# Kernel optimization log

Hardware: AMD Instinct MI355X
Metric: run time of the kernel (lower is better)

## Reference

```python
import jax, jax.numpy as jnp
import numpy as np

B, T, C = 2, 2048, 1024
H, DH = 16, 64          # n_heads = d_model // 64
WIN = 256               # sliding window size
K = 32                  # n_oscillators
DFF = 4096              # d_ff_hidden
NEG = -1e9


def setup_inputs() -> dict:
    key = jax.random.key(0)
    ks = jax.random.split(key, 16)
    sC = 1.0 / np.sqrt(C)
    sF = 1.0 / np.sqrt(DFF)
    sK = 1.0 / np.sqrt(K)
    return {
        "x": jax.random.normal(ks[0], (B, T, C), jnp.float32),
        "norm1_w": jnp.ones((C,), jnp.float32),
        "qkv_w": jax.random.normal(ks[1], (3 * C, C), jnp.float32) * sC,
        "qkv_b": jnp.zeros((3 * C,), jnp.float32),
        "proj_w": jax.random.normal(ks[2], (C, C), jnp.float32) * sC,
        "proj_b": jnp.zeros((C,), jnp.float32),
        "gate_w": jax.random.normal(ks[3], (1, C), jnp.float32) * 0.01,
        "gate_b": jnp.zeros((1,), jnp.float32),
        "trn_win": jax.random.normal(ks[4], (K, C), jnp.float32) * sC,
        "trn_wout": jax.random.normal(ks[5], (C, K), jnp.float32) * sK,
        "trn_gate_w": jax.random.normal(ks[6], (K, C), jnp.float32) * sC,
        "trn_gate_b": jnp.zeros((K,), jnp.float32),
        "trn_a_logit": jax.random.normal(ks[7], (K,), jnp.float32),
        "trn_theta": jax.random.uniform(ks[8], (K,), jnp.float32, 0.0, np.pi),
        "trn_res_scale": jnp.asarray(0.1, jnp.float32),
        "norm2_w": jnp.ones((C,), jnp.float32),
        "ffn_gate_w": jax.random.normal(ks[9], (DFF, C), jnp.float32) * sC,
        "ffn_up_w": jax.random.normal(ks[10], (DFF, C), jnp.float32) * sC,
        "ffn_down_w": jax.random.normal(ks[11], (C, DFF), jnp.float32) * sF,
    }


def _rms(z, w, eps=1e-6):
    return z * jax.lax.rsqrt(jnp.mean(z * z, axis=-1, keepdims=True) + eps) * w


def reference(x, norm1_w, qkv_w, qkv_b, proj_w, proj_b, gate_w, gate_b,
              trn_win, trn_wout, trn_gate_w, trn_gate_b, trn_a_logit,
              trn_theta, trn_res_scale, norm2_w, ffn_gate_w, ffn_up_w,
              ffn_down_w):
    h = _rms(x, norm1_w)

    # ---- windowed causal attention (dense mask, as in the original) ----
    qkv = h @ qkv_w.T + qkv_b                       # [B,T,3C]
    q, k, v = jnp.split(qkv, 3, axis=-1)
    heads = lambda t: t.reshape(B, T, H, DH).transpose(0, 2, 1, 3)  # [B,H,T,DH]
    q, k, v = heads(q), heads(k), heads(v)
    row = jnp.arange(T)[:, None]
    col = jnp.arange(T)[None, :]
    mask = jnp.where((col <= row) & (col >= row - WIN + 1), 0.0, NEG).astype(x.dtype)
    scores = jnp.einsum('bhqd,bhkd->bhqk', q, k) / jnp.sqrt(jnp.asarray(DH, x.dtype))
    attn = jax.nn.softmax(scores + mask, axis=-1)
    ao = jnp.einsum('bhqk,bhkd->bhqd', attn, v).transpose(0, 2, 1, 3).reshape(B, T, C)
    ao = ao @ proj_w.T + proj_b

    # ---- temporal resonance branch: K damped rotating oscillators ----
    u = h @ trn_win.T                               # [B,T,K] drive
    a = jax.nn.sigmoid(trn_a_logit)                 # amplitude in (0,1) (amplitude_max=1)
    ct, st = jnp.cos(trn_theta), jnp.sin(trn_theta)

    def step(carry, ut):
        sr, si = carry
        nsr = a * (ct * sr - st * si) + ut
        nsi = a * (st * sr + ct * si)
        return (nsr, nsi), nsr

    init = (jnp.zeros((B, K), x.dtype), jnp.zeros((B, K), x.dtype))
    _, ys = jax.lax.scan(step, init, u.transpose(1, 0, 2))  # ys: [T,B,K]
    y = ys.transpose(1, 0, 2)                                # [B,T,K]
    tg = jax.nn.sigmoid(h @ trn_gate_w.T + trn_gate_b)
    trn_out = ((tg * y) @ trn_wout.T) * trn_res_scale        # [B,T,C]

    # ---- sigmoid gate mix + residual ----
    g = jax.nn.sigmoid(h @ gate_w.T + gate_b)       # [B,T,1]
    x = x + g * ao + (1.0 - g) * trn_out

    # ---- SwiGLU FFN ----
    h2 = _rms(x, norm2_w)
    ffn = (jax.nn.silu(h2 @ ffn_gate_w.T) * (h2 @ ffn_up_w.T)) @ ffn_down_w.T
    return x + ffn
```

## Files before the change

### kernel.cpp

```cpp
#include <hip/hip_runtime.h>


typedef unsigned short u16;
typedef unsigned short u16x8 __attribute__((ext_vector_type(8)));
typedef __bf16 bf16x8 __attribute__((ext_vector_type(8)));
typedef float f32x4 __attribute__((ext_vector_type(4)));

#define DI static __device__ __forceinline__

DI u16 f2b(float f){
  union { float f; unsigned u; } v; v.f = f;
  unsigned r = v.u + 0x7FFFu + ((v.u >> 16) & 1u);
  return (u16)(r >> 16);
}
DI float b2f(u16 b){
  union { unsigned u; float f; } v; v.u = ((unsigned)b) << 16; return v.f;
}
DI u16x8 ld8(const u16* p){ return *(const u16x8*)p; }

DI f32x4 MFMA16(u16x8 a, u16x8 b, f32x4 c){
  return __builtin_amdgcn_mfma_f32_16x16x32_bf16(
      __builtin_bit_cast(bf16x8, a), __builtin_bit_cast(bf16x8, b), c, 0, 0, 0);
}

DI void async16(const void* g, void* l){
  void* gg = const_cast<void*>(g);
  __builtin_amdgcn_global_load_lds(
      (__attribute__((address_space(1))) void*)gg,
      (__attribute__((address_space(3))) void*)l, 16, 0, 0);
}

__global__ __launch_bounds__(256) void prep_kernel(
    const float* __restrict__ qkvw, const float* __restrict__ projw,
    const float* __restrict__ fgw, const float* __restrict__ fuw,
    const float* __restrict__ fdw, const float* __restrict__ twin,
    const float* __restrict__ tgw, const float* __restrict__ twout,
    u16* __restrict__ dst,
    const float* __restrict__ x, const float* __restrict__ n1w,
    const float* __restrict__ gw, const float* __restrict__ gb,
    u16* __restrict__ h, float* __restrict__ g)
{
  const int blk = blockIdx.x, tid = threadIdx.x;
  if (blk < 16640){
    size_t i = (size_t)blk * 256 + tid;
    if (i >= 4259840u) return;
    size_t e = i * 4;
    float4 v;
    if (e < 3145728u)        v = *(const float4*)(qkvw + e);
    else if (e < 3276800u){
      size_t i2 = e - 3145728u;
      int row = (int)(i2 >> 10), c = (int)(i2 & 1023);
      if (row < 32)      v = *(const float4*)(twin + row * 1024 + c);
      else if (row < 64) v = *(const float4*)(tgw + (row - 32) * 1024 + c);
      else               v = make_float4(0.f, 0.f, 0.f, 0.f);
    }
    else if (e < 4456448u){
      unsigned i2 = (unsigned)(e - 3276800u);
      unsigned row = i2 / 1152u, kk = i2 - row * 1152u;
      if (kk < 1024u)      v = *(const float4*)(projw + (size_t)row * 1024 + kk);
      else if (kk < 1056u) v = *(const float4*)(twout + (size_t)row * 32 + (kk - 1024u));
      else                 v = make_float4(0.f, 0.f, 0.f, 0.f);
    }
    else if (e < 12845056u){
      size_t i2 = e - 4456448u;
      int row = (int)(i2 >> 10), c = (int)(i2 & 1023);
      int G = row >> 5, j = row & 31;
      const float* src = (j < 16) ? fgw : fuw;
      v = *(const float4*)(src + (size_t)(G * 16 + (j & 15)) * 1024 + c);
    }
    else                   v = *(const float4*)(fdw + (e - 12845056u));
    uint2 p;
    p.x = (unsigned)f2b(v.x) | ((unsigned)f2b(v.y) << 16);
    p.y = (unsigned)f2b(v.z) | ((unsigned)f2b(v.w) << 16);
    *(uint2*)(dst + e) = p;
    return;
  }
  const int row = blk - 16640;
  const int wave = tid >> 6, lane = tid & 63;
  __shared__ float sb[8];
  float4 xv = ((const float4*)(x + (size_t)row * 1024))[tid];
  float ss = xv.x*xv.x + xv.y*xv.y + xv.z*xv.z + xv.w*xv.w;
#pragma unroll
  for (int m = 32; m; m >>= 1) ss += __shfl_xor(ss, m);
  if (lane == 0) sb[wave] = ss;
  __syncthreads();
  float rstd = rsqrtf((sb[0]+sb[1]+sb[2]+sb[3]) * (1.f/1024.f) + 1e-6f);
  float4 wv = ((const float4*)n1w)[tid];
  float h0 = xv.x*rstd*wv.x, h1 = xv.y*rstd*wv.y;
  float h2v = xv.z*rstd*wv.z, h3 = xv.w*rstd*wv.w;
  uint2 pk;
  pk.x = (unsigned)f2b(h0) | ((unsigned)f2b(h1) << 16);
  pk.y = (unsigned)f2b(h2v) | ((unsigned)f2b(h3) << 16);
  ((uint2*)(h + (size_t)row * 1024))[tid] = pk;
  float4 gv = ((const float4*)gw)[tid];
  float gd = h0*gv.x + h1*gv.y + h2v*gv.z + h3*gv.w;
#pragma unroll
  for (int m = 32; m; m >>= 1) gd += __shfl_xor(gd, m);
  if (lane == 0) sb[4 + wave] = gd;
  __syncthreads();
  if (tid == 0) g[row] = 1.f / (1.f + __expf(-(sb[4]+sb[5]+sb[6]+sb[7] + gb[0])));
}

__global__ __launch_bounds__(256) void reduce_mix_norm(
    const u16* __restrict__ part, const float* __restrict__ x,
    const float* __restrict__ g, const float* __restrict__ pb,
    const float* __restrict__ n2w,
    float* __restrict__ out, u16* __restrict__ h2)
{
  const int row = blockIdx.x, tid = threadIdx.x;
  const int wave = tid >> 6, lane = tid & 63;
  __shared__ float sb[4];
  const size_t ro = (size_t)row * 1024;
  uint2 a0 = ((const uint2*)(part + ro))[tid];
  uint2 a1 = ((const uint2*)(part + 4194304 + ro))[tid];
  float4 bb = ((const float4*)pb)[tid];
  float4 xv = ((const float4*)(x + ro))[tid];
  float gg = g[row];
  float m0 = xv.x + b2f((u16)a0.x) + b2f((u16)a1.x) + gg*bb.x;
  float m1 = xv.y + b2f((u16)(a0.x >> 16)) + b2f((u16)(a1.x >> 16)) + gg*bb.y;
  float m2 = xv.z + b2f((u16)a0.y) + b2f((u16)a1.y) + gg*bb.z;
  float m3 = xv.w + b2f((u16)(a0.y >> 16)) + b2f((u16)(a1.y >> 16)) + gg*bb.w;
  float4 mo; mo.x = m0; mo.y = m1; mo.z = m2; mo.w = m3;
  ((float4*)(out + ro))[tid] = mo;
  float ss = m0*m0 + m1*m1 + m2*m2 + m3*m3;
#pragma unroll
  for (int m = 32; m; m >>= 1) ss += __shfl_xor(ss, m);
  if (lane == 0) sb[wave] = ss;
  __syncthreads();
  float rstd = rsqrtf((sb[0]+sb[1]+sb[2]+sb[3]) * (1.f/1024.f) + 1e-6f);
  float4 wv = ((const float4*)n2w)[tid];
  uint2 pk;
  pk.x = (unsigned)f2b(m0*rstd*wv.x) | ((unsigned)f2b(m1*rstd*wv.y) << 16);
  pk.y = (unsigned)f2b(m2*rstd*wv.z) | ((unsigned)f2b(m3*rstd*wv.w) << 16);
  ((uint2*)(h2 + ro))[tid] = pk;
}

__global__ __launch_bounds__(256) void reduce_down(
    const u16* __restrict__ part, float* __restrict__ out)
{
  size_t i = (size_t)blockIdx.x * 256 + threadIdx.x;
  uint2 a0 = ((const uint2*)part)[i];
  uint2 a1 = ((const uint2*)(part + 4194304))[i];
  uint2 a2 = ((const uint2*)(part + 8388608))[i];
  uint2 a3 = ((const uint2*)(part + 12582912))[i];
  float4 xv = ((float4*)out)[i];
  float4 o;
  o.x = xv.x + b2f((u16)a0.x) + b2f((u16)a1.x) + b2f((u16)a2.x) + b2f((u16)a3.x);
  o.y = xv.y + b2f((u16)(a0.x >> 16)) + b2f((u16)(a1.x >> 16))
             + b2f((u16)(a2.x >> 16)) + b2f((u16)(a3.x >> 16));
  o.z = xv.z + b2f((u16)a0.y) + b2f((u16)a1.y) + b2f((u16)a2.y) + b2f((u16)a3.y);
  o.w = xv.w + b2f((u16)(a0.y >> 16)) + b2f((u16)(a1.y >> 16))
             + b2f((u16)(a2.y >> 16)) + b2f((u16)(a3.y >> 16));
  ((float4*)out)[i] = o;
}

template<int MODE>
__global__ __launch_bounds__(256) void gemm_bt(
    const u16* __restrict__ A, const u16* __restrict__ B,
    float* __restrict__ outF, float* __restrict__ outF2, u16* __restrict__ outB,
    const float* __restrict__ bias, const float* __restrict__ auxF,
    int M, int N, int K)
{
  __shared__ __align__(16) u16 sA[2][128 * 32];
  __shared__ __align__(16) u16 sB[2][128 * 32];
  const int tid = threadIdx.x;
  const int wave = tid >> 6, lane = tid & 63;
  const int lr = lane & 15, lq = lane >> 4;
  const int m0 = blockIdx.x * 128, n0 = blockIdx.y * 128;
  const int wm = (wave & 1) * 64, wn = (wave >> 1) * 64;
  const int ks = K / (int)gridDim.z;
  const int kbeg = (int)blockIdx.z * ks, kend = kbeg + ks;
  f32x4 acc[4][4] = {};
  const int srow = wave * 16 + (lane >> 2);
  const int scol = (lane & 3) * 8;
  const u16* gA = A + (size_t)(m0 + srow) * K + scol;
  const u16* gB = B + (size_t)(n0 + srow) * K + scol;
  u16* lA0 = &sA[0][(wave * 16) * 32];
  u16* lA1 = &sA[0][(64 + wave * 16) * 32];
  u16* lB0 = &sB[0][(wave * 16) * 32];
  u16* lB1 = &sB[0][(64 + wave * 16) * 32];
  const size_t K64 = (size_t)64 * K;
  const int BUF = 128 * 32;

  for (int k0 = kbeg; k0 < kend; k0 += 64){
    async16(gA + k0,            lA0);
    async16(gA + K64 + k0,      lA1);
    async16(gB + k0,            lB0);
    async16(gB + K64 + k0,      lB1);
    async16(gA + k0 + 32,       lA0 + BUF);
    async16(gA + K64 + k0 + 32, lA1 + BUF);
    async16(gB + k0 + 32,       lB0 + BUF);
    async16(gB + K64 + k0 + 32, lB1 + BUF);
    __syncthreads();
#pragma unroll
    for (int buf = 0; buf < 2; buf++){
      u16x8 af[4], bf[4];
#pragma unroll
      for (int i = 0; i < 4; i++) af[i] = ld8(&sA[buf][(wm + i*16 + lr)*32 + lq*8]);
#pragma unroll
      for (int i = 0; i < 4; i++) bf[i] = ld8(&sB[buf][(wn + i*16 + lr)*32 + lq*8]);
#pragma unroll
      for (int mi = 0; mi < 4; mi++)
#pragma unroll
        for (int ni = 0; ni < 4; ni++)
          acc[mi][ni] = MFMA16(af[mi], bf[ni], acc[mi][ni]);
    }
    __syncthreads();
  }

  if (MODE == 7){
    const int cb = ((n0 + wn) >> 1) + lr;
#pragma unroll
    for (int mi = 0; mi < 4; mi++){
      const int row = m0 + wm + mi*16 + lq*4;
#pragma unroll
      for (int p = 0; p < 2; p++){
        const int col = cb + p*16;
#pragma unroll
        for (int r = 0; r < 4; r++){
          float gv = acc[mi][2*p][r], uv = acc[mi][2*p+1][r];
          float rv = gv / (1.f + __expf(-gv)) * uv;
          outB[(size_t)(row + r) * (N >> 1) + col] = f2b(rv);
        }
      }
    }
    return;
  }

#pragma unroll
  for (int mi = 0; mi < 4; mi++){
    const int row = m0 + wm + mi*16 + lq*4;
#pragma unroll
    for (int ni = 0; ni < 4; ni++){
      const int col = n0 + wn + ni*16 + lr;
#pragma unroll
      for (int r = 0; r < 4; r++){
        const int rr = row + r;
        float v = acc[mi][ni][r];
        if (MODE == 0){
          if (n0 < 3072){
            outB[(size_t)rr * 3072 + col] = f2b(v + bias[col]);
          } else {
            int c2 = col - 3072;
            int bb = rr >> 11, tt = rr & 2047;
            if (c2 < 32) outF[((size_t)bb * 32 + c2) * 2048 + tt] = v;
            else if (c2 < 64)
              outF2[(size_t)rr * 32 + (c2 - 32)] =
                  1.f / (1.f + __expf(-(v + auxF[c2 - 32])));
          }
        } else if (MODE == 9){
          outB[(size_t)blockIdx.z * (size_t)M + (size_t)rr * N + col] = f2b(v);
        }
      }
    }
  }
}

__global__ __launch_bounds__(256) void attn_scan(
    const u16* __restrict__ qkv, const float* __restrict__ g,
    const float* __restrict__ u_t, const float* __restrict__ tg,
    const float* __restrict__ alog, const float* __restrict__ theta,
    const float* __restrict__ tscale, u16* __restrict__ Ap)
{
  __shared__ __align__(16) u16 sVt[64 * 72];
  __shared__ __align__(16) u16 sP[4][16 * 72];
  __shared__ float4 sc[256];
  const int blk = blockIdx.x, tid = threadIdx.x;

  if (blk < 1024){
    const int tile = blk & 31, hh = (blk >> 5) & 15, b = blk >> 9;
    const int t0 = tile * 64;
    const int wave = tid >> 6, lane = tid & 63;
    const int lr = lane & 15, lq = lane >> 4;
    const int qt = t0 + wave * 16;

    const u16* base = qkv + (size_t)b * 2048 * 3072 + hh * 64;
    const u16* qrow = base + (size_t)(qt + lr) * 3072 + lq * 8;
    u16x8 qf0 = ld8(qrow), qf1 = ld8(qrow + 32);
    const u16* kbase = base + 1024;
    const u16* vbase = base + 2048;

    f32x4 o0 = {0,0,0,0}, o1 = {0,0,0,0}, o2 = {0,0,0,0}, o3 = {0,0,0,0};
    float lsum[4] = {0.f, 0.f, 0.f, 0.f};
    const float c1 = 0.125f * 1.44269504088896f;

    const int kb = (t0 >= 256) ? (t0 - 256) : 0;
    const int ntl = (t0 + 64 - kb) >> 6;
    for (int it = 0; it < ntl; ++it){
      const int kt = kb + it * 64;
      __syncthreads();
      {
        const int key = tid & 63, dseg = tid >> 6;
        const u16* gv = vbase + (size_t)(kt + key) * 3072 + dseg * 16;
        u16x8 v0 = ld8(gv), v1 = ld8(gv + 8);
#pragma unroll
        for (int j = 0; j < 8; j++){
          sVt[(dseg*16 + j)     * 72 + key] = v0[j];
          sVt[(dseg*16 + 8 + j) * 72 + key] = v1[j];
        }
      }
      __syncthreads();
      const bool active = (kt < qt + 16) && (kt + 318 >= qt);
      if (!active) continue;

      f32x4 s[4] = {};
#pragma unroll
      for (int gK = 0; gK < 4; gK++){
        const u16* kr = kbase + (size_t)(kt + gK*16 + lr) * 3072 + lq * 8;
        u16x8 k0 = ld8(kr), k1 = ld8(kr + 32);
        s[gK] = MFMA16(qf0, k0, s[gK]);
        s[gK] = MFMA16(qf1, k1, s[gK]);
      }
#pragma unroll
      for (int r = 0; r < 4; r++){
        const int q = qt + lq * 4 + r;
#pragma unroll
        for (int gK = 0; gK < 4; gK++){
          const int c = kt + gK*16 + lr;
          float p = (c <= q && c + 255 >= q) ? exp2f(s[gK][r] * c1) : 0.f;
          lsum[r] += p;
          sP[wave][(lq*4 + r) * 72 + gK*16 + lr] = f2b(p);
        }
      }
      __builtin_amdgcn_s_waitcnt(0xc07f);
      u16x8 pf0 = ld8(&sP[wave][lr * 72 + lq * 8]);
      u16x8 pf1 = ld8(&sP[wave][lr * 72 + 32 + lq * 8]);
      o0 = MFMA16(pf0, ld8(&sVt[(lr)      * 72 + lq * 8]), o0);
      o0 = MFMA16(pf1, ld8(&sVt[(lr)      * 72 + 32 + lq * 8]), o0);
      o1 = MFMA16(pf0, ld8(&sVt[(16 + lr) * 72 + lq * 8]), o1);
      o1 = MFMA16(pf1, ld8(&sVt[(16 + lr) * 72 + 32 + lq * 8]), o1);
      o2 = MFMA16(pf0, ld8(&sVt[(32 + lr) * 72 + lq * 8]), o2);
      o2 = MFMA16(pf1, ld8(&sVt[(32 + lr) * 72 + 32 + lq * 8]), o2);
      o3 = MFMA16(pf0, ld8(&sVt[(48 + lr) * 72 + lq * 8]), o3);
      o3 = MFMA16(pf1, ld8(&sVt[(48 + lr) * 72 + 32 + lq * 8]), o3);
    }

#pragma unroll
    for (int r = 0; r < 4; r++){
      float l = lsum[r];
      l += __shfl_xor(l, 1); l += __shfl_xor(l, 2);
      l += __shfl_xor(l, 4); l += __shfl_xor(l, 8);
      lsum[r] = l;
    }

    const int trow = b * 2048 + qt + lq * 4;
    u16* aor = Ap + (size_t)trow * 1152 + hh * 64 + lr;
#pragma unroll
    for (int r = 0; r < 4; r++){
      float inv = g[trow + r] / lsum[r];
      u16* p = aor + (size_t)r * 1152;
      p[0]  = f2b(o0[r] * inv);
      p[16] = f2b(o1[r] * inv);
      p[32] = f2b(o2[r] * inv);
      p[48] = f2b(o3[r] * inv);
    }
    return;
  }

  if (blk < 1088){
    const int bk = blk - 1024;
    const int b = bk >> 5, k = bk & 31;
    const int j = tid;
    const float a = 1.f / (1.f + __expf(-alog[k]));
    const float th = theta[k];
    const float rs = tscale[0];
    const float wr = a * __cosf(th), wi = a * __sinf(th);
    const float* ubp = u_t + ((size_t)b * 32 + k) * 2048 + j * 8;
    float4 ua = ((const float4*)ubp)[0];
    float4 ub4 = ((const float4*)ubp)[1];
    float ur[8] = {ua.x, ua.y, ua.z, ua.w, ub4.x, ub4.y, ub4.z, ub4.w};
    float sr = 0.f, si = 0.f;
#pragma unroll
    for (int i = 0; i < 8; i++){
      float nr = wr*sr - wi*si + ur[i];
      float ni = wi*sr + wr*si;
      sr = nr; si = ni;
    }
    float w2r = wr*wr - wi*wi, w2i = 2.f*wr*wi;
    float w4r = w2r*w2r - w2i*w2i, w4i = 2.f*w2r*w2i;
    float Ar = w4r*w4r - w4i*w4i, Ai = 2.f*w4r*w4i;
    float4 cur; cur.x = Ar; cur.y = Ai; cur.z = sr; cur.w = si;
    sc[j] = cur;
    __syncthreads();
    for (int s = 1; s < 256; s <<= 1){
      float4 pv;
      const bool has = (j >= s);
      if (has) pv = sc[j - s];
      __syncthreads();
      if (has){
        float nar = cur.x*pv.x - cur.y*pv.y;
        float nai = cur.x*pv.y + cur.y*pv.x;
        float nbr = cur.x*pv.z - cur.y*pv.w + cur.z;
        float nbi = cur.x*pv.w + cur.y*pv.z + cur.w;
        cur.x = nar; cur.y = nai; cur.z = nbr; cur.w = nbi;
      }
      sc[j] = cur;
      __syncthreads();
    }
    float s_r = 0.f, s_i = 0.f;
    if (j > 0){ float4 pr = sc[j - 1]; s_r = pr.z; s_i = pr.w; }
    const int bt0 = b * 2048 + j * 8;
    const float* tgp = tg + (size_t)bt0 * 32 + k;
    u16* zp = Ap + (size_t)bt0 * 1152 + 1024 + k;
#pragma unroll
    for (int i = 0; i < 8; i++){
      float nr = wr*s_r - wi*s_i + ur[i];
      float ni = wi*s_r + wr*s_i;
      s_r = nr; s_i = ni;
      float sc2 = (1.f - g[bt0 + i]) * rs;
      zp[(size_t)i * 1152] = f2b(s_r * tgp[(size_t)i * 32] * sc2);
    }
    return;
  }

  {
    unsigned idx = (unsigned)(blk - 1088) * 256 + tid;
    unsigned row = idx / 12u, seg = idx - row * 12u;
    uint4 z4; z4.x = 0; z4.y = 0; z4.z = 0; z4.w = 0;
    *(uint4*)(Ap + (size_t)row * 1152 + 1056 + seg * 8) = z4;
  }
}

extern "C" void kernel_launch(void* const* d_in, const int* in_sizes, int n_in,
                              void* d_out, int out_size, void* d_ws, size_t ws_size,
                              hipStream_t stream)
{
  (void)in_sizes; (void)n_in; (void)out_size; (void)ws_size;
  const float* x      = (const float*)d_in[0];
  const float* n1w    = (const float*)d_in[1];
  const float* qkvw   = (const float*)d_in[2];
  const float* qkvb   = (const float*)d_in[3];
  const float* projw  = (const float*)d_in[4];
  const float* projb  = (const float*)d_in[5];
  const float* gatew  = (const float*)d_in[6];
  const float* gateb  = (const float*)d_in[7];
  const float* twin   = (const float*)d_in[8];
  const float* twout  = (const float*)d_in[9];
  const float* tgw    = (const float*)d_in[10];
  const float* tgb    = (const float*)d_in[11];
  const float* talog  = (const float*)d_in[12];
  const float* ttheta = (const float*)d_in[13];
  const float* tscale = (const float*)d_in[14];
  const float* n2w    = (const float*)d_in[15];
  const float* fgw    = (const float*)d_in[16];
  const float* fuw    = (const float*)d_in[17];
  const float* fdw    = (const float*)d_in[18];
  float* out = (float*)d_out;

  char* wsb = (char*)d_ws;
  size_t off = 0;
  auto take = [&](size_t bytes) -> void* {
    void* r = wsb + off; off += (bytes + 255) & ~(size_t)255; return r;
  };
  u16*   wall = (u16*)take(17039360ull * 2);
  u16*   h    = (u16*)take(4194304ull * 2);
  u16*   h2   = (u16*)take(4194304ull * 2);
  float* g    = (float*)take(4096ull * 4);
  float* u_t  = (float*)take(131072ull * 4);
  float* tg   = (float*)take(131072ull * 4);
  u16*   regA = (u16*)take(4096ull * 4096 * 2);
  u16*   regB = (u16*)take(4096ull * 4096 * 2);

  u16* wq  = wall;
  u16* wpx = wall + 3276800;
  u16* wgu = wall + 4456448;
  u16* wd  = wall + 12845056;
  u16* qkv    = regA;
  u16* pproj  = regA;
  u16* pdown  = regA;
  u16* Ap     = regB;
  u16* act    = regB;

  prep_kernel<<<20736, 256, 0, stream>>>(qkvw, projw, fgw, fuw, fdw, twin, tgw,
                                         twout, wall, x, n1w, gatew, gateb, h, g);
  gemm_bt<0><<<dim3(32, 25), 256, 0, stream>>>(h, wq, u_t, tg, qkv, qkvb,
                                               tgb, 0, 3200, 1024);
  attn_scan<<<1280, 256, 0, stream>>>(qkv, g, u_t, tg, talog, ttheta, tscale, Ap);
  gemm_bt<9><<<dim3(32, 8, 2), 256, 0, stream>>>(Ap, wpx, nullptr, nullptr, pproj,
                                                 nullptr, nullptr, 4194304, 1024, 1152);
  reduce_mix_norm<<<4096, 256, 0, stream>>>(pproj, x, g, projb, n2w, out, h2);
  gemm_bt<7><<<dim3(32, 64), 256, 0, stream>>>(h2, wgu, nullptr, nullptr, act, nullptr,
                                               nullptr, 0, 8192, 1024);
  gemm_bt<9><<<dim3(32, 8, 4), 256, 0, stream>>>(act, wd, nullptr, nullptr, pdown,
                                                 nullptr, nullptr, 4194304, 1024, 4096);
  reduce_down<<<4096, 256, 0, stream>>>(pdown, out);
}
```

Baseline: 408.3 us.

## Overlap FFN weight conversion with QKV GEMM and halve down-proj split-K

```diff
diff --git a/kernel.cpp b/kernel.cpp
--- a/kernel.cpp
+++ b/kernel.cpp
@@ -32,18 +32,15 @@
 
 __global__ __launch_bounds__(256) void prep_kernel(
     const float* __restrict__ qkvw, const float* __restrict__ projw,
-    const float* __restrict__ fgw, const float* __restrict__ fuw,
-    const float* __restrict__ fdw, const float* __restrict__ twin,
-    const float* __restrict__ tgw, const float* __restrict__ twout,
-    u16* __restrict__ dst,
+    const float* __restrict__ twin, const float* __restrict__ tgw,
+    const float* __restrict__ twout, u16* __restrict__ dst,
     const float* __restrict__ x, const float* __restrict__ n1w,
     const float* __restrict__ gw, const float* __restrict__ gb,
     u16* __restrict__ h, float* __restrict__ g)
 {
   const int blk = blockIdx.x, tid = threadIdx.x;
-  if (blk < 16640){
+  if (blk < 4352){
     size_t i = (size_t)blk * 256 + tid;
-    if (i >= 4259840u) return;
     size_t e = i * 4;
     float4 v;
     if (e < 3145728u)        v = *(const float4*)(qkvw + e);
@@ -54,28 +51,20 @@
       else if (row < 64) v = *(const float4*)(tgw + (row - 32) * 1024 + c);
       else               v = make_float4(0.f, 0.f, 0.f, 0.f);
     }
-    else if (e < 4456448u){
+    else {
       unsigned i2 = (unsigned)(e - 3276800u);
       unsigned row = i2 / 1152u, kk = i2 - row * 1152u;
       if (kk < 1024u)      v = *(const float4*)(projw + (size_t)row * 1024 + kk);
       else if (kk < 1056u) v = *(const float4*)(twout + (size_t)row * 32 + (kk - 1024u));
       else                 v = make_float4(0.f, 0.f, 0.f, 0.f);
     }
-    else if (e < 12845056u){
-      size_t i2 = e - 4456448u;
-      int row = (int)(i2 >> 10), c = (int)(i2 & 1023);
-      int G = row >> 5, j = row & 31;
-      const float* src = (j < 16) ? fgw : fuw;
-      v = *(const float4*)(src + (size_t)(G * 16 + (j & 15)) * 1024 + c);
-    }
-    else                   v = *(const float4*)(fdw + (e - 12845056u));
     uint2 p;
     p.x = (unsigned)f2b(v.x) | ((unsigned)f2b(v.y) << 16);
     p.y = (unsigned)f2b(v.z) | ((unsigned)f2b(v.w) << 16);
     *(uint2*)(dst + e) = p;
     return;
   }
-  const int row = blk - 16640;
+  const int row = blk - 4352;
   const int wave = tid >> 6, lane = tid & 63;
   __shared__ float sb[8];
   float4 xv = ((const float4*)(x + (size_t)row * 1024))[tid];
@@ -141,16 +130,12 @@
   size_t i = (size_t)blockIdx.x * 256 + threadIdx.x;
   uint2 a0 = ((const uint2*)part)[i];
   uint2 a1 = ((const uint2*)(part + 4194304))[i];
-  uint2 a2 = ((const uint2*)(part + 8388608))[i];
-  uint2 a3 = ((const uint2*)(part + 12582912))[i];
   float4 xv = ((float4*)out)[i];
   float4 o;
-  o.x = xv.x + b2f((u16)a0.x) + b2f((u16)a1.x) + b2f((u16)a2.x) + b2f((u16)a3.x);
-  o.y = xv.y + b2f((u16)(a0.x >> 16)) + b2f((u16)(a1.x >> 16))
-             + b2f((u16)(a2.x >> 16)) + b2f((u16)(a3.x >> 16));
-  o.z = xv.z + b2f((u16)a0.y) + b2f((u16)a1.y) + b2f((u16)a2.y) + b2f((u16)a3.y);
-  o.w = xv.w + b2f((u16)(a0.y >> 16)) + b2f((u16)(a1.y >> 16))
-             + b2f((u16)(a2.y >> 16)) + b2f((u16)(a3.y >> 16));
+  o.x = xv.x + b2f((u16)a0.x) + b2f((u16)a1.x);
+  o.y = xv.y + b2f((u16)(a0.x >> 16)) + b2f((u16)(a1.x >> 16));
+  o.z = xv.z + b2f((u16)a0.y) + b2f((u16)a1.y);
+  o.w = xv.w + b2f((u16)(a0.y >> 16)) + b2f((u16)(a1.y >> 16));
   ((float4*)out)[i] = o;
 }
 
@@ -159,8 +144,36 @@
     const u16* __restrict__ A, const u16* __restrict__ B,
     float* __restrict__ outF, float* __restrict__ outF2, u16* __restrict__ outB,
     const float* __restrict__ bias, const float* __restrict__ auxF,
+    const float* __restrict__ cf0, const float* __restrict__ cf1,
+    const float* __restrict__ cf2, u16* __restrict__ cdst,
     int M, int N, int K)
 {
+  if (MODE == 0 && blockIdx.z == 1){
+    const int c = (int)blockIdx.x + (int)blockIdx.y * 32;
+    const int t = threadIdx.x;
+#pragma unroll
+    for (int i = 0; i < 16; i++){
+      unsigned q = (unsigned)c * 4096u + (unsigned)i * 256u + (unsigned)t;
+      if (q >= 3145728u) break;
+      size_t e = 4456448u + (size_t)q * 4;
+      float4 v;
+      if (e < 12845056u){
+        unsigned i2 = (unsigned)(e - 4456448u);
+        int row = (int)(i2 >> 10), col = (int)(i2 & 1023);
+        int G = row >> 5, j = row & 31;
+        const float* src = (j < 16) ? cf0 : cf1;
+        v = *(const float4*)(src + (size_t)(G * 16 + (j & 15)) * 1024 + col);
+      } else {
+        v = *(const float4*)(cf2 + (e - 12845056u));
+      }
+      uint2 p;
+      p.x = (unsigned)f2b(v.x) | ((unsigned)f2b(v.y) << 16);
+      p.y = (unsigned)f2b(v.z) | ((unsigned)f2b(v.w) << 16);
+      *(uint2*)(cdst + e) = p;
+    }
+    return;
+  }
+
   __shared__ __align__(16) u16 sA[2][128 * 32];
   __shared__ __align__(16) u16 sB[2][128 * 32];
   const int tid = threadIdx.x;
@@ -168,8 +181,10 @@
   const int lr = lane & 15, lq = lane >> 4;
   const int m0 = blockIdx.x * 128, n0 = blockIdx.y * 128;
   const int wm = (wave & 1) * 64, wn = (wave >> 1) * 64;
-  const int ks = K / (int)gridDim.z;
-  const int kbeg = (int)blockIdx.z * ks, kend = kbeg + ks;
+  const int gz = (MODE == 0) ? 1 : (int)gridDim.z;
+  const int ks = K / gz;
+  const int kbeg = (MODE == 0) ? 0 : (int)blockIdx.z * ks;
+  const int kend = kbeg + ks;
   f32x4 acc[4][4] = {};
   const int srow = wave * 16 + (lane >> 2);
   const int scol = (lane & 3) * 8;
@@ -267,8 +282,9 @@
   __shared__ float4 sc[256];
   const int blk = blockIdx.x, tid = threadIdx.x;
 
-  if (blk < 1024){
-    const int tile = blk & 31, hh = (blk >> 5) & 15, b = blk >> 9;
+  if (blk >= 256){
+    const int ablk = blk - 256;
+    const int tile = ablk & 31, hh = (ablk >> 5) & 15, b = ablk >> 9;
     const int t0 = tile * 64;
     const int wave = tid >> 6, lane = tid & 63;
     const int lr = lane & 15, lq = lane >> 4;
@@ -357,9 +373,8 @@
     return;
   }
 
-  if (blk < 1088){
-    const int bk = blk - 1024;
-    const int b = bk >> 5, k = bk & 31;
+  if (blk < 64){
+    const int b = blk >> 5, k = blk & 31;
     const int j = tid;
     const float a = 1.f / (1.f + __expf(-alog[k]));
     const float th = theta[k];
@@ -414,7 +429,7 @@
   }
 
   {
-    unsigned idx = (unsigned)(blk - 1088) * 256 + tid;
+    unsigned idx = (unsigned)(blk - 64) * 256 + tid;
     unsigned row = idx / 12u, seg = idx - row * 12u;
     uint4 z4; z4.x = 0; z4.y = 0; z4.z = 0; z4.w = 0;
     *(uint4*)(Ap + (size_t)row * 1152 + 1056 + seg * 8) = z4;
@@ -471,17 +486,21 @@
   u16* Ap     = regB;
   u16* act    = regB;
 
-  prep_kernel<<<20736, 256, 0, stream>>>(qkvw, projw, fgw, fuw, fdw, twin, tgw,
-                                         twout, wall, x, n1w, gatew, gateb, h, g);
-  gemm_bt<0><<<dim3(32, 25), 256, 0, stream>>>(h, wq, u_t, tg, qkv, qkvb,
-                                               tgb, 0, 3200, 1024);
+  prep_kernel<<<8448, 256, 0, stream>>>(qkvw, projw, twin, tgw, twout, wall,
+                                        x, n1w, gatew, gateb, h, g);
+  gemm_bt<0><<<dim3(32, 25, 2), 256, 0, stream>>>(h, wq, u_t, tg, qkv, qkvb,
+                                                  tgb, fgw, fuw, fdw, wall,
+                                                  0, 3200, 1024);
   attn_scan<<<1280, 256, 0, stream>>>(qkv, g, u_t, tg, talog, ttheta, tscale, Ap);
   gemm_bt<9><<<dim3(32, 8, 2), 256, 0, stream>>>(Ap, wpx, nullptr, nullptr, pproj,
+                                                 nullptr, nullptr, nullptr, nullptr,
                                                  nullptr, nullptr, 4194304, 1024, 1152);
   reduce_mix_norm<<<4096, 256, 0, stream>>>(pproj, x, g, projb, n2w, out, h2);
   gemm_bt<7><<<dim3(32, 64), 256, 0, stream>>>(h2, wgu, nullptr, nullptr, act, nullptr,
+                                               nullptr, nullptr, nullptr, nullptr,
                                                nullptr, 0, 8192, 1024);
-  gemm_bt<9><<<dim3(32, 8, 4), 256, 0, stream>>>(act, wd, nullptr, nullptr, pdown,
+  gemm_bt<9><<<dim3(32, 8, 2), 256, 0, stream>>>(act, wd, nullptr, nullptr, pdown,
+                                                 nullptr, nullptr, nullptr, nullptr,
                                                  nullptr, nullptr, 4194304, 1024, 4096);
   reduce_down<<<4096, 256, 0, stream>>>(pdown, out);
 }
```

After: 415.2 us. No clear change (+1.7%).
